# Optimization experiments

Measured on AMD Instinct MI355X. Metric: run time of the kernel, lower is better.

## Reference

```python
import jax, jax.numpy as jnp
import numpy as np

B, OBS, GENC, H, C, NF = 16384, 512, 216, 1024, 64, 8
IN = GENC + OBS + OBS  # use_state=True: [graph, state, next_state]


def setup_inputs() -> dict:
    key = jax.random.key(0)
    ks = jax.random.split(key, 9)
    graph = jax.random.randint(ks[0], (B, GENC), 0, 2).astype(jnp.float32)
    state = jax.random.normal(ks[1], (B, OBS), dtype=jnp.float32)
    next_state = jax.random.normal(ks[2], (B, OBS), dtype=jnp.float32)
    W1 = jax.random.normal(ks[3], (NF, IN, H), dtype=jnp.float32) * 0.02
    b1 = jnp.zeros((NF, H), dtype=jnp.float32)
    W2 = jax.random.normal(ks[4], (NF, H, H), dtype=jnp.float32) * 0.02
    b2 = jnp.zeros((NF, H), dtype=jnp.float32)
    W3 = jax.random.normal(ks[5], (NF, H, C), dtype=jnp.float32) * 0.02
    b3 = jnp.zeros((NF, C), dtype=jnp.float32)
    return {"graph": graph, "state": state, "next_state": next_state,
            "W1": W1, "b1": b1, "W2": W2, "b2": b2, "W3": W3, "b3": b3}


def reference(graph, state, next_state, W1, b1, W2, b2, W3, b3):
    # wide_diayn forward: concat input, run per-factor MLP on rows where
    # graph[:, i] == 1, later factors overwrite earlier; unmatched rows -> 0.
    x = jnp.concatenate([graph, state, next_state], axis=-1)  # [B, IN]
    nf = W1.shape[0]
    mask = graph[:, :nf] == 1.0  # [B, F] per-factor indicator
    h = jax.nn.relu(jnp.einsum('bi,fih->bfh', x, W1) + b1[None, :, :])
    h = jax.nn.relu(jnp.einsum('bfh,fhg->bfg', h, W2) + b2[None, :, :])
    out_all = jnp.einsum('bfg,fgc->bfc', h, W3) + b3[None, :, :]  # [B, F, C]
    rev_first = jnp.argmax(mask[:, ::-1].astype(jnp.int32), axis=1)
    last_idx = (nf - 1) - rev_first  # [B]
    sel = jnp.take_along_axis(out_all, last_idx[:, None, None], axis=1)[:, 0, :]
    any_active = mask.any(axis=1)
    return jnp.where(any_active[:, None], sel, jnp.zeros_like(sel))
```

## Files before the change

kernel.cpp:

```cpp
#include <hip/hip_runtime.h>

#define BB   16384
#define GENC 216
#define OBS  512
#define NH   1024
#define NC   64
#define NFAC 8
#define NIN  1240
#define KP1  1280
#define MTILES 136

typedef __attribute__((ext_vector_type(4))) float f32x4;
typedef __attribute__((ext_vector_type(8))) short short8;
typedef __attribute__((ext_vector_type(4))) short short4v;

__device__ __forceinline__ unsigned short f2bf(float f) {
  union { float f; unsigned u; } x; x.f = f;
  unsigned r = x.u + 0x7fffu + ((x.u >> 16) & 1u);
  return (unsigned short)(r >> 16);
}

__device__ __forceinline__ void gl_lds16(const unsigned short* g, unsigned short* l) {
  __builtin_amdgcn_global_load_lds(
      (const __attribute__((address_space(1))) void*)g,
      (__attribute__((address_space(3))) void*)l, 16, 0, 0);
}

__device__ __forceinline__ int xcd_chunk(int gid, int nwg) {
  int q = nwg >> 3, r = nwg & 7, x = gid & 7, p = gid >> 3;
  return (x < r ? x * (q + 1) : r * (q + 1) + (x - r) * q) + p;
}

__global__ void bucket_kernel(const float* __restrict__ graph,
                              int* __restrict__ cnt, int* __restrict__ rowlist) {
  __shared__ int lcnt[NFAC];
  __shared__ int lbase[NFAC];
  int tid = threadIdx.x;
  if (tid < NFAC) lcnt[tid] = 0;
  __syncthreads();
  int b = blockIdx.x * 256 + tid;
  const float* g = graph + (size_t)b * GENC;
  float4 g0 = *(const float4*)g;
  float4 g1 = *(const float4*)(g + 4);
  int f = -1;
  if (g0.x == 1.f) f = 0;
  if (g0.y == 1.f) f = 1;
  if (g0.z == 1.f) f = 2;
  if (g0.w == 1.f) f = 3;
  if (g1.x == 1.f) f = 4;
  if (g1.y == 1.f) f = 5;
  if (g1.z == 1.f) f = 6;
  if (g1.w == 1.f) f = 7;
  int li = 0;
  if (f >= 0) li = atomicAdd(&lcnt[f], 1);
  __syncthreads();
  if (tid < NFAC) lbase[tid] = lcnt[tid] ? atomicAdd(&cnt[tid], lcnt[tid]) : 0;
  __syncthreads();
  if (f >= 0) rowlist[f * BB + lbase[f] + li] = b;
}

__global__ void gather_x(const float* __restrict__ graph,
                         const float* __restrict__ state,
                         const float* __restrict__ nexts,
                         const int* __restrict__ cnt,
                         const int* __restrict__ rowlist,
                         unsigned short* __restrict__ xg) {
  int w = threadIdx.x >> 6, lane = threadIdx.x & 63;
  int pos = blockIdx.x * 4 + w;
  int f = -1, loc = 0, acc = 0;
#pragma unroll
  for (int i = 0; i < NFAC; ++i) {
    int c = cnt[i];
    if (f < 0 && pos < acc + c) { f = i; loc = pos - acc; }
    acc += c;
  }
  if (f < 0) return;
  int b = rowlist[f * BB + loc];
  unsigned short* dst = xg + (size_t)pos * KP1;
#pragma unroll
  for (int it = 0; it < 5; ++it) {
    int c = it * 64 + lane;
    float4 v;
    if (c < 54)       v = *(const float4*)(graph + (size_t)b * GENC + c * 4);
    else if (c < 182) v = *(const float4*)(state + (size_t)b * OBS + (c - 54) * 4);
    else if (c < 310) v = *(const float4*)(nexts + (size_t)b * OBS + (c - 182) * 4);
    else              v = make_float4(0.f, 0.f, 0.f, 0.f);
    short4v s;
    s[0] = (short)f2bf(v.x); s[1] = (short)f2bf(v.y);
    s[2] = (short)f2bf(v.z); s[3] = (short)f2bf(v.w);
    *(short4v*)(dst + c * 4) = s;
  }
}

__global__ void transpose_all(const float* __restrict__ W1,
                              const float* __restrict__ W2,
                              const float* __restrict__ W3,
                              unsigned short* __restrict__ w1t,
                              unsigned short* __restrict__ w2t,
                              unsigned short* __restrict__ w3t) {
  __shared__ unsigned short tile[64][65];
  int z = blockIdx.z;
  const float* src; unsigned short* dst; int K, N, KPad;
  if (z < 8)        { src = W1 + (size_t)z * NIN * NH;       dst = w1t + (size_t)z * NH * KP1; K = NIN; N = NH; KPad = KP1; }
  else if (z < 16)  { src = W2 + (size_t)(z - 8) * NH * NH;  dst = w2t + (size_t)(z - 8) * NH * NH; K = NH; N = NH; KPad = NH; }
  else              { src = W3 + (size_t)(z - 16) * NH * NC; dst = w3t + (size_t)(z - 16) * NC * NH; K = NH; N = NC; KPad = NH; }
  int k0 = blockIdx.y * 64, n0 = blockIdx.x * 64;
  if (k0 >= KPad || n0 >= N) return;
  int tr = threadIdx.x >> 6, tc = threadIdx.x & 63;
#pragma unroll
  for (int i = 0; i < 16; ++i) {
    int r = i * 4 + tr;
    int k = k0 + r;
    float v = (k < K) ? src[(size_t)k * N + n0 + tc] : 0.0f;
    tile[r][tc] = f2bf(v);
  }
  __syncthreads();
  int kp = threadIdx.x & 31, nb = threadIdx.x >> 5;
#pragma unroll
  for (int i = 0; i < 8; ++i) {
    int n = i * 8 + nb;
    union { short2 s2; unsigned u; } v;
    v.s2.x = (short)tile[kp * 2][n];
    v.s2.y = (short)tile[kp * 2 + 1][n];
    *(unsigned*)(dst + (size_t)(n0 + n) * KPad + k0 + kp * 2) = v.u;
  }
}

template <int LAYER>
__launch_bounds__(512, 2)
__global__ void mlp_gemm_big(const unsigned short* __restrict__ Abase,
                             const unsigned short* __restrict__ Wt,
                             const float* __restrict__ bias,
                             unsigned short* __restrict__ Hout,
                             const int* __restrict__ cnt) {
  constexpr int K  = (LAYER == 1) ? KP1 : NH;
  constexpr int NT = K / 64;
  constexpr int NB = NH / 256;

  extern __shared__ unsigned short smem[];

  const int wg = xcd_chunk(blockIdx.x, MTILES * NB);
  const int ty = wg / NB;
  const int n0 = (wg % NB) * 256;

  int f = -1, m0 = 0, goff = 0, cntf = 0;
  {
    int acc = 0, off = 0;
#pragma unroll
    for (int i = 0; i < NFAC; ++i) {
      int c = cnt[i];
      int t = (c + 127) >> 7;
      if (f < 0 && ty < acc + t) { f = i; m0 = (ty - acc) * 128; goff = off; cntf = c; }
      acc += t; off += c;
    }
  }
  if (f < 0) return;

  const int tid = threadIdx.x, wid = tid >> 6, lane = tid & 63;
  const int wm = wid >> 2, wn = wid & 3;

  const int sr = tid >> 3;
  const int sc = (tid & 7) ^ (sr & 7);
  const unsigned short* pu[6];
  {
    const unsigned short* Ao = Abase + (size_t)(goff + m0) * K;
    const unsigned short* Bo = Wt + (size_t)f * NH * K + (size_t)n0 * K;
    pu[0] = Ao + (size_t)sr * K + sc * 8;
    pu[1] = Ao + (size_t)(64 + sr) * K + sc * 8;
#pragma unroll
    for (int u = 0; u < 4; ++u) pu[2 + u] = Bo + (size_t)(u * 64 + sr) * K + sc * 8;
  }
  const int dst8 = tid * 8;

  unsigned short* A0 = smem;              unsigned short* B0 = smem + 8192;
  unsigned short* A1 = smem + 24576;      unsigned short* B1 = A1 + 8192;
  unsigned short* A2 = smem + 49152;      unsigned short* B2 = A2 + 8192;

  f32x4 acc[4][4];
#pragma unroll
  for (int a = 0; a < 4; ++a)
#pragma unroll
    for (int b = 0; b < 4; ++b) acc[a][b] = (f32x4){0.f, 0.f, 0.f, 0.f};

  auto stage = [&](unsigned short* Ab, unsigned short* Bb) {
    gl_lds16(pu[0], Ab + dst8);        pu[0] += 64;
    gl_lds16(pu[1], Ab + 4096 + dst8); pu[1] += 64;
#pragma unroll
    for (int u = 0; u < 4; ++u) { gl_lds16(pu[2 + u], Bb + u * 4096 + dst8); pu[2 + u] += 64; }
  };

  stage(A0, B0);
  stage(A1, B1);
  unsigned short *Ac = A0, *Bc = B0, *An = A1, *Bn = B1, *Af = A2, *Bf = B2;

#pragma unroll 1
  for (int t = 0; t < NT; ++t) {
    if (t < NT - 1) { asm volatile("s_waitcnt vmcnt(6)" ::: "memory"); }
    else            { asm volatile("s_waitcnt vmcnt(0)" ::: "memory"); }
    __builtin_amdgcn_sched_barrier(0);
    __builtin_amdgcn_s_barrier();
    __builtin_amdgcn_sched_barrier(0);

    short8 av[4][2], bv[4][2];
#pragma unroll
    for (int nf = 0; nf < 4; ++nf) {
      int c = wn * 64 + nf * 16 + (lane & 15);
#pragma unroll
      for (int ks = 0; ks < 2; ++ks) {
        int kc = ks * 4 + (lane >> 4);
        bv[nf][ks] = *(const short8*)(Bc + c * 64 + ((kc ^ (c & 7)) << 3));
      }
    }
#pragma unroll
    for (int mf = 0; mf < 4; ++mf) {
      int r = wm * 64 + mf * 16 + (lane & 15);
#pragma unroll
      for (int ks = 0; ks < 2; ++ks) {
        int kc = ks * 4 + (lane >> 4);
        av[mf][ks] = *(const short8*)(Ac + r * 64 + ((kc ^ (r & 7)) << 3));
      }
    }
    if (t + 2 < NT) stage(Af, Bf);
    __builtin_amdgcn_s_setprio(1);
#pragma unroll
    for (int mf = 0; mf < 4; ++mf)
#pragma unroll
      for (int nf = 0; nf < 4; ++nf)
#pragma unroll
        for (int ks = 0; ks < 2; ++ks)
          acc[mf][nf] = __builtin_amdgcn_mfma_f32_16x16x32_bf16(
              av[mf][ks], bv[nf][ks], acc[mf][nf], 0, 0, 0);
    __builtin_amdgcn_s_setprio(0);
    unsigned short* ta = Ac; unsigned short* tb = Bc;
    Ac = An; Bc = Bn; An = Af; Bn = Bf; Af = ta; Bf = tb;
  }

  const float* bs = bias + f * NH;
#pragma unroll
  for (int nf = 0; nf < 4; ++nf) {
    int col = n0 + wn * 64 + nf * 16 + (lane & 15);
    float bvv = bs[col];
#pragma unroll
    for (int mf = 0; mf < 4; ++mf) {
      int rbase = wm * 64 + mf * 16 + ((lane >> 4) << 2);
#pragma unroll
      for (int i = 0; i < 4; ++i) {
        int pos = m0 + rbase + i;
        if (pos < cntf) {
          float v = fmaxf(acc[mf][nf][i] + bvv, 0.0f);
          Hout[(size_t)(goff + pos) * NH + col] = f2bf(v);
        }
      }
    }
  }
}

__launch_bounds__(256, 2)
__global__ void mlp_gemm3(const unsigned short* __restrict__ Abase,
                          const unsigned short* __restrict__ Wt,
                          const float* __restrict__ bias,
                          float* __restrict__ Out,
                          const int* __restrict__ cnt,
                          const int* __restrict__ rowlist) {
  constexpr int K = NH;
  constexpr int NKT = K / 64;

  const int wg = xcd_chunk(blockIdx.x, MTILES);
  const int ty = wg;

  int f = -1, m0 = 0, goff = 0, cntf = 0;
  {
    int acc = 0, off = 0;
#pragma unroll
    for (int i = 0; i < NFAC; ++i) {
      int c = cnt[i];
      int t = (c + 127) >> 7;
      if (f < 0 && ty < acc + t) { f = i; m0 = (ty - acc) * 128; goff = off; cntf = c; }
      acc += t; off += c;
    }
  }
  if (f < 0) return;

  __shared__ unsigned short As[2][128 * 64];
  __shared__ unsigned short Bs[2][64 * 64];

  const int tid = threadIdx.x;
  const int wid = tid >> 6, lane = tid & 63;

  const int rl = lane >> 3;
  const int chs = (lane & 7) ^ rl;
  const unsigned short* pA[4];
  const unsigned short* pB[2];
  {
    const unsigned short* Aorg = Abase + (size_t)(goff + m0) * K;
    const unsigned short* Borg = Wt + (size_t)f * NC * K;
#pragma unroll
    for (int i = 0; i < 4; ++i)
      pA[i] = Aorg + (size_t)(wid * 32 + i * 8 + rl) * K + chs * 8;
#pragma unroll
    for (int i = 0; i < 2; ++i)
      pB[i] = Borg + (size_t)(wid * 16 + i * 8 + rl) * K + chs * 8;
  }

  f32x4 acc[2][4];
#pragma unroll
  for (int a = 0; a < 2; ++a)
#pragma unroll
    for (int b = 0; b < 4; ++b) acc[a][b] = (f32x4){0.f, 0.f, 0.f, 0.f};

  auto stage = [&](int buf) {
#pragma unroll
    for (int i = 0; i < 4; ++i) {
      gl_lds16(pA[i], &As[buf][(wid * 32 + i * 8) * 64]);
      pA[i] += 64;
    }
#pragma unroll
    for (int i = 0; i < 2; ++i) {
      gl_lds16(pB[i], &Bs[buf][(wid * 16 + i * 8) * 64]);
      pB[i] += 64;
    }
  };

  auto compute = [&](int buf) {
#pragma unroll
    for (int ks = 0; ks < 2; ++ks) {
      const int kc8 = ks * 4 + (lane >> 4);
      short8 av[2], bv[4];
#pragma unroll
      for (int mf = 0; mf < 2; ++mf) {
        int row = wid * 32 + mf * 16 + (lane & 15);
        av[mf] = *(const short8*)(&As[buf][0] + row * 64 + ((kc8 ^ (row & 7)) << 3));
      }
#pragma unroll
      for (int nf = 0; nf < 4; ++nf) {
        int col = nf * 16 + (lane & 15);
        bv[nf] = *(const short8*)(&Bs[buf][0] + col * 64 + ((kc8 ^ (col & 7)) << 3));
      }
      __builtin_amdgcn_s_setprio(1);
#pragma unroll
      for (int mf = 0; mf < 2; ++mf)
#pragma unroll
        for (int nf = 0; nf < 4; ++nf)
          acc[mf][nf] = __builtin_amdgcn_mfma_f32_16x16x32_bf16(
              av[mf], bv[nf], acc[mf][nf], 0, 0, 0);
      __builtin_amdgcn_s_setprio(0);
    }
  };

  stage(0);
  stage(1);
#pragma unroll 1
  for (int kt = 0; kt < NKT; ++kt) {
    if (kt < NKT - 1) { asm volatile("s_waitcnt vmcnt(6)" ::: "memory"); }
    else              { asm volatile("s_waitcnt vmcnt(0)" ::: "memory"); }
    __builtin_amdgcn_sched_barrier(0);
    __builtin_amdgcn_s_barrier();
    __builtin_amdgcn_sched_barrier(0);
    compute(kt & 1);
    __builtin_amdgcn_sched_barrier(0);
    __builtin_amdgcn_s_barrier();
    __builtin_amdgcn_sched_barrier(0);
    if (kt + 2 < NKT) stage(kt & 1);
  }

  const float* bs = bias + f * NC;
#pragma unroll
  for (int nf = 0; nf < 4; ++nf) {
    int col = nf * 16 + (lane & 15);
    float bvv = bs[col];
#pragma unroll
    for (int mf = 0; mf < 2; ++mf) {
      int rbase = wid * 32 + mf * 16 + ((lane >> 4) << 2);
#pragma unroll
      for (int i = 0; i < 4; ++i) {
        int pos = m0 + rbase + i;
        if (pos < cntf) {
          int b = rowlist[f * BB + pos];
          Out[(size_t)b * NC + col] = acc[mf][nf][i] + bvv;
        }
      }
    }
  }
}

extern "C" void kernel_launch(void* const* d_in, const int* in_sizes, int n_in,
                              void* d_out, int out_size, void* d_ws, size_t ws_size,
                              hipStream_t stream) {
  const float* graph = (const float*)d_in[0];
  const float* state = (const float*)d_in[1];
  const float* nexts = (const float*)d_in[2];
  const float* W1 = (const float*)d_in[3];
  const float* b1 = (const float*)d_in[4];
  const float* W2 = (const float*)d_in[5];
  const float* b2 = (const float*)d_in[6];
  const float* W3 = (const float*)d_in[7];
  const float* b3 = (const float*)d_in[8];
  float* out = (float*)d_out;
  char* ws = (char*)d_ws;

  const size_t ROWCAP = BB + 256;
  const size_t OFF_ROW = 256;
  const size_t OFF_W1T = OFF_ROW + (size_t)NFAC * BB * 4;
  const size_t OFF_W2T = OFF_W1T + (size_t)NFAC * NH * KP1 * 2;
  const size_t OFF_W3T = OFF_W2T + (size_t)NFAC * NH * NH * 2;
  const size_t OFF_H1  = OFF_W3T + (size_t)NFAC * NC * NH * 2;
  const size_t OFF_XG  = OFF_H1 + ROWCAP * NH * 2;

  int* cnt = (int*)ws;
  int* rowlist = (int*)(ws + OFF_ROW);
  unsigned short* w1t = (unsigned short*)(ws + OFF_W1T);
  unsigned short* w2t = (unsigned short*)(ws + OFF_W2T);
  unsigned short* w3t = (unsigned short*)(ws + OFF_W3T);
  unsigned short* h1  = (unsigned short*)(ws + OFF_H1);
  unsigned short* xg  = (unsigned short*)(ws + OFF_XG);
  unsigned short* h2  = xg;

  hipFuncSetAttribute(reinterpret_cast<const void*>(mlp_gemm_big<1>),
                      hipFuncAttributeMaxDynamicSharedMemorySize, 147456);
  hipFuncSetAttribute(reinterpret_cast<const void*>(mlp_gemm_big<2>),
                      hipFuncAttributeMaxDynamicSharedMemorySize, 147456);

  hipMemsetAsync(cnt, 0, 64, stream);
  hipMemsetAsync(d_out, 0, (size_t)out_size * sizeof(float), stream);

  bucket_kernel<<<BB / 256, 256, 0, stream>>>(graph, cnt, rowlist);
  gather_x<<<BB / 4, 256, 0, stream>>>(graph, state, nexts, cnt, rowlist, xg);
  transpose_all<<<dim3(16, 20, 24), 256, 0, stream>>>(W1, W2, W3, w1t, w2t, w3t);

  mlp_gemm_big<1><<<MTILES * 4, 512, 147456, stream>>>(xg, w1t, b1, h1, cnt);
  mlp_gemm_big<2><<<MTILES * 4, 512, 147456, stream>>>(h1, w2t, b2, h2, cnt);
  mlp_gemm3<<<MTILES, 256, 0, stream>>>(h2, w3t, b3, out, cnt, rowlist);
}
```

Before: 243.2 us.

## Widen layer-1/2 GEMM tile to 128x512 with split double-buffered staging

Result: slower. 275.9 us (+13.5%).

```diff
diff --git a/kernel.cpp b/kernel.cpp
--- a/kernel.cpp
+++ b/kernel.cpp
@@ -135,13 +135,13 @@
                              const int* __restrict__ cnt) {
   constexpr int K  = (LAYER == 1) ? KP1 : NH;
   constexpr int NT = K / 64;
-  constexpr int NB = NH / 256;
+  constexpr int NB = NH / 512;
 
   extern __shared__ unsigned short smem[];
 
   const int wg = xcd_chunk(blockIdx.x, MTILES * NB);
   const int ty = wg / NB;
-  const int n0 = (wg % NB) * 256;
+  const int n0 = (wg % NB) * 512;
 
   int f = -1, m0 = 0, goff = 0, cntf = 0;
   {
@@ -157,92 +157,144 @@
   if (f < 0) return;
 
   const int tid = threadIdx.x, wid = tid >> 6, lane = tid & 63;
-  const int wm = wid >> 2, wn = wid & 3;
 
   const int sr = tid >> 3;
   const int sc = (tid & 7) ^ (sr & 7);
-  const unsigned short* pu[6];
+  const unsigned short* pA[2];
+  const unsigned short* pB[8];
   {
     const unsigned short* Ao = Abase + (size_t)(goff + m0) * K;
     const unsigned short* Bo = Wt + (size_t)f * NH * K + (size_t)n0 * K;
-    pu[0] = Ao + (size_t)sr * K + sc * 8;
-    pu[1] = Ao + (size_t)(64 + sr) * K + sc * 8;
-#pragma unroll
-    for (int u = 0; u < 4; ++u) pu[2 + u] = Bo + (size_t)(u * 64 + sr) * K + sc * 8;
+    pA[0] = Ao + (size_t)sr * K + sc * 8;
+    pA[1] = Ao + (size_t)(64 + sr) * K + sc * 8;
+#pragma unroll
+    for (int u = 0; u < 8; ++u) pB[u] = Bo + (size_t)(u * 64 + sr) * K + sc * 8;
   }
   const int dst8 = tid * 8;
 
-  unsigned short* A0 = smem;              unsigned short* B0 = smem + 8192;
-  unsigned short* A1 = smem + 24576;      unsigned short* B1 = A1 + 8192;
-  unsigned short* A2 = smem + 49152;      unsigned short* B2 = A2 + 8192;
-
-  f32x4 acc[4][4];
-#pragma unroll
-  for (int a = 0; a < 4; ++a)
+  f32x4 acc[8][4];
+#pragma unroll
+  for (int a = 0; a < 8; ++a)
 #pragma unroll
     for (int b = 0; b < 4; ++b) acc[a][b] = (f32x4){0.f, 0.f, 0.f, 0.f};
 
-  auto stage = [&](unsigned short* Ab, unsigned short* Bb) {
-    gl_lds16(pu[0], Ab + dst8);        pu[0] += 64;
-    gl_lds16(pu[1], Ab + 4096 + dst8); pu[1] += 64;
-#pragma unroll
-    for (int u = 0; u < 4; ++u) { gl_lds16(pu[2 + u], Bb + u * 4096 + dst8); pu[2 + u] += 64; }
+  auto stageA = [&](unsigned short* Ab) {
+    gl_lds16(pA[0], Ab + dst8);        pA[0] += 64;
+    gl_lds16(pA[1], Ab + 4096 + dst8); pA[1] += 64;
   };
-
-  stage(A0, B0);
-  stage(A1, B1);
-  unsigned short *Ac = A0, *Bc = B0, *An = A1, *Bn = B1, *Af = A2, *Bf = B2;
+  auto stageB1 = [&](unsigned short* Bb) {
+#pragma unroll
+    for (int u = 0; u < 4; ++u) { gl_lds16(pB[u], Bb + u * 4096 + dst8); pB[u] += 64; }
+  };
+  auto stageB2 = [&](unsigned short* Bb) {
+#pragma unroll
+    for (int u = 4; u < 8; ++u) { gl_lds16(pB[u], Bb + u * 4096 + dst8); pB[u] += 64; }
+  };
+
+  stageA(smem);
+  stageB1(smem + 8192);
+  stageB2(smem + 8192);
 
 #pragma unroll 1
   for (int t = 0; t < NT; ++t) {
-    if (t < NT - 1) { asm volatile("s_waitcnt vmcnt(6)" ::: "memory"); }
-    else            { asm volatile("s_waitcnt vmcnt(0)" ::: "memory"); }
+    unsigned short* Ab = smem + (t & 1) * 40960;
+    unsigned short* Bb = Ab + 8192;
+    unsigned short* An = smem + ((t & 1) ^ 1) * 40960;
+    unsigned short* Bn = An + 8192;
+
+    asm volatile("s_waitcnt vmcnt(0)" ::: "memory");
     __builtin_amdgcn_sched_barrier(0);
     __builtin_amdgcn_s_barrier();
     __builtin_amdgcn_sched_barrier(0);
 
-    short8 av[4][2], bv[4][2];
-#pragma unroll
-    for (int nf = 0; nf < 4; ++nf) {
-      int c = wn * 64 + nf * 16 + (lane & 15);
+    short8 alo[4][2], ahi[4][2], b0[2][2], b1[2][2];
+#pragma unroll
+    for (int mf = 0; mf < 4; ++mf) {
+      int r = mf * 16 + (lane & 15);
 #pragma unroll
       for (int ks = 0; ks < 2; ++ks) {
         int kc = ks * 4 + (lane >> 4);
-        bv[nf][ks] = *(const short8*)(Bc + c * 64 + ((kc ^ (c & 7)) << 3));
-      }
-    }
-#pragma unroll
-    for (int mf = 0; mf < 4; ++mf) {
-      int r = wm * 64 + mf * 16 + (lane & 15);
+        alo[mf][ks] = *(const short8*)(Ab + r * 64 + ((kc ^ (r & 7)) << 3));
+      }
+    }
+#pragma unroll
+    for (int nf = 0; nf < 2; ++nf) {
+      int c = wid * 64 + nf * 16 + (lane & 15);
 #pragma unroll
       for (int ks = 0; ks < 2; ++ks) {
         int kc = ks * 4 + (lane >> 4);
-        av[mf][ks] = *(const short8*)(Ac + r * 64 + ((kc ^ (r & 7)) << 3));
-      }
-    }
-    if (t + 2 < NT) stage(Af, Bf);
+        b0[nf][ks] = *(const short8*)(Bb + c * 64 + ((kc ^ (c & 7)) << 3));
+      }
+    }
+#pragma unroll
+    for (int nf = 0; nf < 2; ++nf) {
+      int c = wid * 64 + (nf + 2) * 16 + (lane & 15);
+#pragma unroll
+      for (int ks = 0; ks < 2; ++ks) {
+        int kc = ks * 4 + (lane >> 4);
+        b1[nf][ks] = *(const short8*)(Bb + c * 64 + ((kc ^ (c & 7)) << 3));
+      }
+    }
+    if (t + 1 < NT) { stageA(An); stageB1(Bn); }
+
     __builtin_amdgcn_s_setprio(1);
 #pragma unroll
     for (int mf = 0; mf < 4; ++mf)
 #pragma unroll
-      for (int nf = 0; nf < 4; ++nf)
+      for (int nf = 0; nf < 2; ++nf)
 #pragma unroll
         for (int ks = 0; ks < 2; ++ks)
           acc[mf][nf] = __builtin_amdgcn_mfma_f32_16x16x32_bf16(
-              av[mf][ks], bv[nf][ks], acc[mf][nf], 0, 0, 0);
+              alo[mf][ks], b0[nf][ks], acc[mf][nf], 0, 0, 0);
     __builtin_amdgcn_s_setprio(0);
-    unsigned short* ta = Ac; unsigned short* tb = Bc;
-    Ac = An; Bc = Bn; An = Af; Bn = Bf; Af = ta; Bf = tb;
+
+#pragma unroll
+    for (int mf = 0; mf < 4; ++mf) {
+      int r = (mf + 4) * 16 + (lane & 15);
+#pragma unroll
+      for (int ks = 0; ks < 2; ++ks) {
+        int kc = ks * 4 + (lane >> 4);
+        ahi[mf][ks] = *(const short8*)(Ab + r * 64 + ((kc ^ (r & 7)) << 3));
+      }
+    }
+    if (t + 1 < NT) stageB2(Bn);
+
+    __builtin_amdgcn_s_setprio(1);
+#pragma unroll
+    for (int mf = 0; mf < 4; ++mf)
+#pragma unroll
+      for (int nf = 0; nf < 2; ++nf)
+#pragma unroll
+        for (int ks = 0; ks < 2; ++ks)
+          acc[mf][nf + 2] = __builtin_amdgcn_mfma_f32_16x16x32_bf16(
+              alo[mf][ks], b1[nf][ks], acc[mf][nf + 2], 0, 0, 0);
+#pragma unroll
+    for (int mf = 0; mf < 4; ++mf)
+#pragma unroll
+      for (int nf = 0; nf < 2; ++nf)
+#pragma unroll
+        for (int ks = 0; ks < 2; ++ks)
+          acc[mf + 4][nf] = __builtin_amdgcn_mfma_f32_16x16x32_bf16(
+              ahi[mf][ks], b0[nf][ks], acc[mf + 4][nf], 0, 0, 0);
+#pragma unroll
+    for (int mf = 0; mf < 4; ++mf)
+#pragma unroll
+      for (int nf = 0; nf < 2; ++nf)
+#pragma unroll
+        for (int ks = 0; ks < 2; ++ks)
+          acc[mf + 4][nf + 2] = __builtin_amdgcn_mfma_f32_16x16x32_bf16(
+              ahi[mf][ks], b1[nf][ks], acc[mf + 4][nf + 2], 0, 0, 0);
+    __builtin_amdgcn_s_setprio(0);
   }
 
   const float* bs = bias + f * NH;
 #pragma unroll
   for (int nf = 0; nf < 4; ++nf) {
-    int col = n0 + wn * 64 + nf * 16 + (lane & 15);
+    int col = n0 + wid * 64 + nf * 16 + (lane & 15);
     float bvv = bs[col];
 #pragma unroll
-    for (int mf = 0; mf < 4; ++mf) {
-      int rbase = wm * 64 + mf * 16 + ((lane >> 4) << 2);
+    for (int mf = 0; mf < 8; ++mf) {
+      int rbase = mf * 16 + ((lane >> 4) << 2);
 #pragma unroll
       for (int i = 0; i < 4; ++i) {
         int pos = m0 + rbase + i;
@@ -416,9 +468,9 @@
   unsigned short* h2  = xg;
 
   hipFuncSetAttribute(reinterpret_cast<const void*>(mlp_gemm_big<1>),
-                      hipFuncAttributeMaxDynamicSharedMemorySize, 147456);
+                      hipFuncAttributeMaxDynamicSharedMemorySize, 163840);
   hipFuncSetAttribute(reinterpret_cast<const void*>(mlp_gemm_big<2>),
-                      hipFuncAttributeMaxDynamicSharedMemorySize, 147456);
+                      hipFuncAttributeMaxDynamicSharedMemorySize, 163840);
 
   hipMemsetAsync(cnt, 0, 64, stream);
   hipMemsetAsync(d_out, 0, (size_t)out_size * sizeof(float), stream);
@@ -427,7 +479,7 @@
   gather_x<<<BB / 4, 256, 0, stream>>>(graph, state, nexts, cnt, rowlist, xg);
   transpose_all<<<dim3(16, 20, 24), 256, 0, stream>>>(W1, W2, W3, w1t, w2t, w3t);
 
-  mlp_gemm_big<1><<<MTILES * 4, 512, 147456, stream>>>(xg, w1t, b1, h1, cnt);
-  mlp_gemm_big<2><<<MTILES * 4, 512, 147456, stream>>>(h1, w2t, b2, h2, cnt);
+  mlp_gemm_big<1><<<MTILES * 2, 512, 163840, stream>>>(xg, w1t, b1, h1, cnt);
+  mlp_gemm_big<2><<<MTILES * 2, 512, 163840, stream>>>(h1, w2t, b2, h2, cnt);
   mlp_gemm3<<<MTILES, 256, 0, stream>>>(h2, w3t, b3, out, cnt, rowlist);
 }
```

## Enlarge layer-1/2 GEMM tiles to 256x256 with 4-phase double-buffered pipeline

Applied to the files above, without the earlier changes.

Measured after the change: 264.2 us. 8.7% more time.

```diff
diff --git a/kernel.cpp b/kernel.cpp
--- a/kernel.cpp
+++ b/kernel.cpp
@@ -9,6 +9,7 @@
 #define NIN  1240
 #define KP1  1280
 #define MTILES 136
+#define MT256  72
 
 typedef __attribute__((ext_vector_type(4))) float f32x4;
 typedef __attribute__((ext_vector_type(8))) short short8;
@@ -128,18 +129,18 @@
 
 template <int LAYER>
 __launch_bounds__(512, 2)
-__global__ void mlp_gemm_big(const unsigned short* __restrict__ Abase,
-                             const unsigned short* __restrict__ Wt,
-                             const float* __restrict__ bias,
-                             unsigned short* __restrict__ Hout,
-                             const int* __restrict__ cnt) {
+__global__ void mlp_gemm8p(const unsigned short* __restrict__ Abase,
+                           const unsigned short* __restrict__ Wt,
+                           const float* __restrict__ bias,
+                           unsigned short* __restrict__ Hout,
+                           const int* __restrict__ cnt) {
   constexpr int K  = (LAYER == 1) ? KP1 : NH;
   constexpr int NT = K / 64;
   constexpr int NB = NH / 256;
 
   extern __shared__ unsigned short smem[];
 
-  const int wg = xcd_chunk(blockIdx.x, MTILES * NB);
+  const int wg = xcd_chunk(blockIdx.x, MT256 * NB);
   const int ty = wg / NB;
   const int n0 = (wg % NB) * 256;
 
@@ -149,8 +150,8 @@
 #pragma unroll
     for (int i = 0; i < NFAC; ++i) {
       int c = cnt[i];
-      int t = (c + 127) >> 7;
-      if (f < 0 && ty < acc + t) { f = i; m0 = (ty - acc) * 128; goff = off; cntf = c; }
+      int t = (c + 255) >> 8;
+      if (f < 0 && ty < acc + t) { f = i; m0 = (ty - acc) * 256; goff = off; cntf = c; }
       acc += t; off += c;
     }
   }
@@ -161,78 +162,166 @@
 
   const int sr = tid >> 3;
   const int sc = (tid & 7) ^ (sr & 7);
-  const unsigned short* pu[6];
+  const unsigned short* pu[8];
   {
     const unsigned short* Ao = Abase + (size_t)(goff + m0) * K;
     const unsigned short* Bo = Wt + (size_t)f * NH * K + (size_t)n0 * K;
-    pu[0] = Ao + (size_t)sr * K + sc * 8;
-    pu[1] = Ao + (size_t)(64 + sr) * K + sc * 8;
-#pragma unroll
-    for (int u = 0; u < 4; ++u) pu[2 + u] = Bo + (size_t)(u * 64 + sr) * K + sc * 8;
+#pragma unroll
+    for (int u = 0; u < 4; ++u) pu[u] = Ao + (size_t)(u * 64 + sr) * K + sc * 8;
+#pragma unroll
+    for (int u = 0; u < 4; ++u) pu[4 + u] = Bo + (size_t)(u * 64 + sr) * K + sc * 8;
   }
   const int dst8 = tid * 8;
 
-  unsigned short* A0 = smem;              unsigned short* B0 = smem + 8192;
-  unsigned short* A1 = smem + 24576;      unsigned short* B1 = A1 + 8192;
-  unsigned short* A2 = smem + 49152;      unsigned short* B2 = A2 + 8192;
-
-  f32x4 acc[4][4];
-#pragma unroll
-  for (int a = 0; a < 4; ++a)
+  f32x4 acc[8][4];
+#pragma unroll
+  for (int a = 0; a < 8; ++a)
 #pragma unroll
     for (int b = 0; b < 4; ++b) acc[a][b] = (f32x4){0.f, 0.f, 0.f, 0.f};
 
-  auto stage = [&](unsigned short* Ab, unsigned short* Bb) {
-    gl_lds16(pu[0], Ab + dst8);        pu[0] += 64;
-    gl_lds16(pu[1], Ab + 4096 + dst8); pu[1] += 64;
-#pragma unroll
-    for (int u = 0; u < 4; ++u) { gl_lds16(pu[2 + u], Bb + u * 4096 + dst8); pu[2 + u] += 64; }
-  };
-
-  stage(A0, B0);
-  stage(A1, B1);
-  unsigned short *Ac = A0, *Bc = B0, *An = A1, *Bn = B1, *Af = A2, *Bf = B2;
+  auto sA = [&](unsigned short* buf, int u) { gl_lds16(pu[u], buf + u * 4096 + dst8); pu[u] += 64; };
+  auto sB = [&](unsigned short* buf, int u) { gl_lds16(pu[4 + u], buf + 16384 + u * 4096 + dst8); pu[4 + u] += 64; };
+
+  sB(smem, 0); sB(smem, 1); sB(smem, 2); sB(smem, 3);
+  sA(smem, 0); sA(smem, 2); sA(smem, 1); sA(smem, 3);
+  asm volatile("s_waitcnt vmcnt(2)" ::: "memory");
+  __builtin_amdgcn_sched_barrier(0);
+  __builtin_amdgcn_s_barrier();
+  __builtin_amdgcn_sched_barrier(0);
+
+  short8 bfr[4][2];
 
 #pragma unroll 1
   for (int t = 0; t < NT; ++t) {
-    if (t < NT - 1) { asm volatile("s_waitcnt vmcnt(6)" ::: "memory"); }
-    else            { asm volatile("s_waitcnt vmcnt(0)" ::: "memory"); }
-    __builtin_amdgcn_sched_barrier(0);
-    __builtin_amdgcn_s_barrier();
-    __builtin_amdgcn_sched_barrier(0);
-
-    short8 av[4][2], bv[4][2];
-#pragma unroll
-    for (int nf = 0; nf < 4; ++nf) {
-      int c = wn * 64 + nf * 16 + (lane & 15);
-#pragma unroll
-      for (int ks = 0; ks < 2; ++ks) {
-        int kc = ks * 4 + (lane >> 4);
-        bv[nf][ks] = *(const short8*)(Bc + c * 64 + ((kc ^ (c & 7)) << 3));
-      }
-    }
-#pragma unroll
-    for (int mf = 0; mf < 4; ++mf) {
-      int r = wm * 64 + mf * 16 + (lane & 15);
-#pragma unroll
-      for (int ks = 0; ks < 2; ++ks) {
-        int kc = ks * 4 + (lane >> 4);
-        av[mf][ks] = *(const short8*)(Ac + r * 64 + ((kc ^ (r & 7)) << 3));
-      }
-    }
-    if (t + 2 < NT) stage(Af, Bf);
-    __builtin_amdgcn_s_setprio(1);
-#pragma unroll
-    for (int mf = 0; mf < 4; ++mf)
-#pragma unroll
-      for (int nf = 0; nf < 4; ++nf)
-#pragma unroll
-        for (int ks = 0; ks < 2; ++ks)
-          acc[mf][nf] = __builtin_amdgcn_mfma_f32_16x16x32_bf16(
-              av[mf][ks], bv[nf][ks], acc[mf][nf], 0, 0, 0);
-    __builtin_amdgcn_s_setprio(0);
-    unsigned short* ta = Ac; unsigned short* tb = Bc;
-    Ac = An; Bc = Bn; An = Af; Bn = Bf; Af = ta; Bf = tb;
+    unsigned short* Ab = smem + (t & 1) * 32768;
+    unsigned short* Bb = Ab + 16384;
+    unsigned short* Nb = smem + ((t + 1) & 1) * 32768;
+    const bool pf = (t + 1 < NT);
+
+    {
+      short8 afr[2][2];
+#pragma unroll
+      for (int nf = 0; nf < 4; ++nf) {
+        int c = wn * 64 + nf * 16 + (lane & 15);
+#pragma unroll
+        for (int ks = 0; ks < 2; ++ks) {
+          int kc = ks * 4 + (lane >> 4);
+          bfr[nf][ks] = *(const short8*)(Bb + c * 64 + ((kc ^ (c & 7)) << 3));
+        }
+      }
+#pragma unroll
+      for (int m2 = 0; m2 < 2; ++m2) {
+        int r = wm * 128 + m2 * 16 + (lane & 15);
+#pragma unroll
+        for (int ks = 0; ks < 2; ++ks) {
+          int kc = ks * 4 + (lane >> 4);
+          afr[m2][ks] = *(const short8*)(Ab + r * 64 + ((kc ^ (r & 7)) << 3));
+        }
+      }
+      if (pf) { sB(Nb, 0); sB(Nb, 1); }
+      __builtin_amdgcn_sched_barrier(0);
+      __builtin_amdgcn_s_barrier();
+      __builtin_amdgcn_sched_barrier(0);
+      asm volatile("s_waitcnt lgkmcnt(0)" ::: "memory");
+      __builtin_amdgcn_sched_barrier(0);
+      __builtin_amdgcn_s_setprio(1);
+#pragma unroll
+      for (int m2 = 0; m2 < 2; ++m2)
+#pragma unroll
+        for (int nf = 0; nf < 4; ++nf)
+#pragma unroll
+          for (int ks = 0; ks < 2; ++ks)
+            acc[m2][nf] = __builtin_amdgcn_mfma_f32_16x16x32_bf16(
+                afr[m2][ks], bfr[nf][ks], acc[m2][nf], 0, 0, 0);
+      __builtin_amdgcn_s_setprio(0);
+    }
+    {
+      short8 afr[2][2];
+#pragma unroll
+      for (int m2 = 0; m2 < 2; ++m2) {
+        int r = wm * 128 + (2 + m2) * 16 + (lane & 15);
+#pragma unroll
+        for (int ks = 0; ks < 2; ++ks) {
+          int kc = ks * 4 + (lane >> 4);
+          afr[m2][ks] = *(const short8*)(Ab + r * 64 + ((kc ^ (r & 7)) << 3));
+        }
+      }
+      if (pf) { sB(Nb, 2); sB(Nb, 3); }
+      if (pf) { asm volatile("s_waitcnt vmcnt(4)" ::: "memory"); }
+      else    { asm volatile("s_waitcnt vmcnt(0)" ::: "memory"); }
+      __builtin_amdgcn_sched_barrier(0);
+      __builtin_amdgcn_s_barrier();
+      __builtin_amdgcn_sched_barrier(0);
+      asm volatile("s_waitcnt lgkmcnt(0)" ::: "memory");
+      __builtin_amdgcn_sched_barrier(0);
+      __builtin_amdgcn_s_setprio(1);
+#pragma unroll
+      for (int m2 = 0; m2 < 2; ++m2)
+#pragma unroll
+        for (int nf = 0; nf < 4; ++nf)
+#pragma unroll
+          for (int ks = 0; ks < 2; ++ks)
+            acc[2 + m2][nf] = __builtin_amdgcn_mfma_f32_16x16x32_bf16(
+                afr[m2][ks], bfr[nf][ks], acc[2 + m2][nf], 0, 0, 0);
+      __builtin_amdgcn_s_setprio(0);
+    }
+    {
+      short8 afr[2][2];
+#pragma unroll
+      for (int m2 = 0; m2 < 2; ++m2) {
+        int r = wm * 128 + (4 + m2) * 16 + (lane & 15);
+#pragma unroll
+        for (int ks = 0; ks < 2; ++ks) {
+          int kc = ks * 4 + (lane >> 4);
+          afr[m2][ks] = *(const short8*)(Ab + r * 64 + ((kc ^ (r & 7)) << 3));
+        }
+      }
+      if (pf) { sA(Nb, 0); sA(Nb, 2); }
+      __builtin_amdgcn_sched_barrier(0);
+      __builtin_amdgcn_s_barrier();
+      __builtin_amdgcn_sched_barrier(0);
+      asm volatile("s_waitcnt lgkmcnt(0)" ::: "memory");
+      __builtin_amdgcn_sched_barrier(0);
+      __builtin_amdgcn_s_setprio(1);
+#pragma unroll
+      for (int m2 = 0; m2 < 2; ++m2)
+#pragma unroll
+        for (int nf = 0; nf < 4; ++nf)
+#pragma unroll
+          for (int ks = 0; ks < 2; ++ks)
+            acc[4 + m2][nf] = __builtin_amdgcn_mfma_f32_16x16x32_bf16(
+                afr[m2][ks], bfr[nf][ks], acc[4 + m2][nf], 0, 0, 0);
+      __builtin_amdgcn_s_setprio(0);
+    }
+    {
+      short8 afr[2][2];
+#pragma unroll
+      for (int m2 = 0; m2 < 2; ++m2) {
+        int r = wm * 128 + (6 + m2) * 16 + (lane & 15);
+#pragma unroll
+        for (int ks = 0; ks < 2; ++ks) {
+          int kc = ks * 4 + (lane >> 4);
+          afr[m2][ks] = *(const short8*)(Ab + r * 64 + ((kc ^ (r & 7)) << 3));
+        }
+      }
+      if (pf) { sA(Nb, 1); sA(Nb, 3); }
+      if (pf) { asm volatile("s_waitcnt vmcnt(2)" ::: "memory"); }
+      __builtin_amdgcn_sched_barrier(0);
+      __builtin_amdgcn_s_barrier();
+      __builtin_amdgcn_sched_barrier(0);
+      asm volatile("s_waitcnt lgkmcnt(0)" ::: "memory");
+      __builtin_amdgcn_sched_barrier(0);
+      __builtin_amdgcn_s_setprio(1);
+#pragma unroll
+      for (int m2 = 0; m2 < 2; ++m2)
+#pragma unroll
+        for (int nf = 0; nf < 4; ++nf)
+#pragma unroll
+          for (int ks = 0; ks < 2; ++ks)
+            acc[6 + m2][nf] = __builtin_amdgcn_mfma_f32_16x16x32_bf16(
+                afr[m2][ks], bfr[nf][ks], acc[6 + m2][nf], 0, 0, 0);
+      __builtin_amdgcn_s_setprio(0);
+    }
   }
 
   const float* bs = bias + f * NH;
@@ -241,8 +330,8 @@
     int col = n0 + wn * 64 + nf * 16 + (lane & 15);
     float bvv = bs[col];
 #pragma unroll
-    for (int mf = 0; mf < 4; ++mf) {
-      int rbase = wm * 64 + mf * 16 + ((lane >> 4) << 2);
+    for (int mf = 0; mf < 8; ++mf) {
+      int rbase = wm * 128 + mf * 16 + ((lane >> 4) << 2);
 #pragma unroll
       for (int i = 0; i < 4; ++i) {
         int pos = m0 + rbase + i;
@@ -415,10 +504,10 @@
   unsigned short* xg  = (unsigned short*)(ws + OFF_XG);
   unsigned short* h2  = xg;
 
-  hipFuncSetAttribute(reinterpret_cast<const void*>(mlp_gemm_big<1>),
-                      hipFuncAttributeMaxDynamicSharedMemorySize, 147456);
-  hipFuncSetAttribute(reinterpret_cast<const void*>(mlp_gemm_big<2>),
-                      hipFuncAttributeMaxDynamicSharedMemorySize, 147456);
+  hipFuncSetAttribute(reinterpret_cast<const void*>(mlp_gemm8p<1>),
+                      hipFuncAttributeMaxDynamicSharedMemorySize, 131072);
+  hipFuncSetAttribute(reinterpret_cast<const void*>(mlp_gemm8p<2>),
+                      hipFuncAttributeMaxDynamicSharedMemorySize, 131072);
 
   hipMemsetAsync(cnt, 0, 64, stream);
   hipMemsetAsync(d_out, 0, (size_t)out_size * sizeof(float), stream);
@@ -427,7 +516,7 @@
   gather_x<<<BB / 4, 256, 0, stream>>>(graph, state, nexts, cnt, rowlist, xg);
   transpose_all<<<dim3(16, 20, 24), 256, 0, stream>>>(W1, W2, W3, w1t, w2t, w3t);
 
-  mlp_gemm_big<1><<<MTILES * 4, 512, 147456, stream>>>(xg, w1t, b1, h1, cnt);
-  mlp_gemm_big<2><<<MTILES * 4, 512, 147456, stream>>>(h1, w2t, b2, h2, cnt);
+  mlp_gemm8p<1><<<MT256 * 4, 512, 131072, stream>>>(xg, w1t, b1, h1, cnt);
+  mlp_gemm8p<2><<<MT256 * 4, 512, 131072, stream>>>(h1, w2t, b2, h2, cnt);
   mlp_gemm3<<<MTILES, 256, 0, stream>>>(h2, w3t, b3, out, cnt, rowlist);
 }
```
